# Kernel optimization log

Hardware: AMD Instinct MI355X
Metric: run time of the kernel (lower is better)

The kernel has to match this reference:

```python
import jax, jax.numpy as jnp
import numpy as np

# --- quantization helpers (I-BERT-style symmetric quantization) ---

def _quant_int(x, scale, bit):
    # round(x/scale) clamped to signed `bit`-bit range (SymmetricQuantFunction)
    n = 2 ** (bit - 1) - 1
    return jnp.clip(jnp.round(x / scale), -n - 1, n)


def quant_linear(x, s_x, W, b, weight_bit=8):
    """QuantLinear: per-output-channel symmetric 8-bit weight quant, int GEMM, dequant.
    Returns (output, bias_scaling_factor[out_features])."""
    n = 2 ** (weight_bit - 1) - 1
    w_scale = jnp.maximum(jnp.max(jnp.abs(W), axis=1), 1e-8) / n          # (out,)
    w_int = _quant_int(W, w_scale[:, None], weight_bit)                   # int-valued (out,in)
    b_scale = w_scale * s_x                                               # (out,) broadcasts with scalar s_x
    b_int = jnp.round(b / b_scale)                                        # 32-bit bias, no clamp needed
    x_int = x / s_x                                                       # int-valued activations
    out_int = jnp.einsum('bsi,oi->bso', x_int, w_int) + b_int
    return out_int * b_scale, b_scale


def quant_act(x, bit):
    """QuantAct: per-tensor symmetric requantization to `bit` bits (dynamic min/max)."""
    n = 2 ** (bit - 1) - 1
    scale = jnp.maximum(jnp.max(jnp.abs(x)), 1e-8) / n                    # scalar
    x_int = _quant_int(x, scale, bit)
    return x_int * scale, scale


def int_gelu(x, s):
    """IntGELU (I-BERT): integer 2nd-order polynomial approximation of erf."""
    k = 1.4142
    c0, c1 = -0.2888, -1.769
    c2 = 1.0 / c0
    SHIFT = 14  # 'const' in the original code

    x_int = x / s
    se = s / k  # scaling factor fed to int_erf
    # --- int_erf ---
    b_int = jnp.floor(c1 / se)
    c_int = jnp.floor(c2 / se ** 2)
    sign = jnp.sign(x_int)
    abs_int = jnp.minimum(jnp.abs(x_int), -b_int)
    y_int = sign * ((abs_int + b_int) ** 2 + c_int)
    se2 = se ** 2 * c0
    y_int = jnp.floor(y_int / 2 ** SHIFT)
    se2 = se2 * 2 ** SHIFT
    # --- gelu = x * (erf/2 + 1/2) in integer form ---
    shift_int = jnp.floor(1.0 / se2)
    out_int = x_int * (y_int + shift_int)
    s_out = s * se2 / 2
    return out_int * s_out, s_out


def setup_inputs() -> dict:
    key = jax.random.key(0)
    k_x, k_w1, k_b1, k_w2, k_b2 = jax.random.split(key, 5)
    B, S, D, H = 8, 1024, 768, 3072
    x = jax.random.normal(k_x, (B, S, D), dtype=jnp.float32)
    act_scaling_factor = jnp.full((1,), 0.02, dtype=jnp.float32)
    # pre-quantize x onto its input grid (x arrives already quantized in the real pipeline)
    x = jnp.round(x / act_scaling_factor) * act_scaling_factor
    W1 = jax.random.normal(k_w1, (H, D), dtype=jnp.float32) * 0.02
    b1 = jax.random.normal(k_b1, (H,), dtype=jnp.float32) * 0.02
    W2 = jax.random.normal(k_w2, (D, H), dtype=jnp.float32) * 0.02
    b2 = jax.random.normal(k_b2, (D,), dtype=jnp.float32) * 0.02
    return {"x": x, "act_scaling_factor": act_scaling_factor,
            "W1": W1, "b1": b1, "W2": W2, "b2": b2}


def reference(x, act_scaling_factor, W1, b1, W2, b2):
    s = act_scaling_factor
    h, s = quant_linear(x, s, W1, b1)       # fc1: int8 GEMM + dequant
    h, s = quant_act(h, 8)                  # qact_gelu
    h, s = int_gelu(h, s)                   # IntGELU
    h, s = quant_act(h, 8)                  # qact1 (drop=0.0 -> identity)
    h, s = quant_linear(h, s, W2, b2)       # fc2
    h, s = quant_act(h, 16)                 # qact2 (16-bit)
    return h, s
```

## Files before the change

### kernel.cpp

```cpp
#include <hip/hip_runtime.h>

typedef _Float16 half8  __attribute__((ext_vector_type(8)));
typedef _Float16 half4v __attribute__((ext_vector_type(4)));
typedef float f32x4 __attribute__((ext_vector_type(4)));
typedef int int4v __attribute__((ext_vector_type(4)));

#define M_DIM 8192
#define D_DIM 768
#define H_DIM 3072

#define WS_WSCALE2   16
#define WS_BINT1     (WS_WSCALE2 + 768*4)
#define WS_BSCALE1   (WS_BINT1 + 3072*4)
#define WS_BINT2     (WS_BSCALE1 + 3072*4)
#define WS_BSCALE2   (WS_BINT2 + 768*4)
#define WS_XQ        34560UL
#define WS_WQ1       (WS_XQ  + (size_t)M_DIM*D_DIM*2)
#define WS_WQ2I      (WS_WQ1 + (size_t)H_DIM*D_DIM*2)
#define WS_H1        (WS_WQ2I + (size_t)D_DIM*H_DIM)
#define WS_Q2        WS_H1
#define WS_H2        (WS_H1 + (size_t)M_DIM*H_DIM)
#define WS_Q1        (WS_H1 + (size_t)M_DIM*H_DIM*4)

__device__ __forceinline__ void gl_lds16(const _Float16* g, _Float16* l) {
  __builtin_amdgcn_global_load_lds(
      (const __attribute__((address_space(1))) void*)g,
      (__attribute__((address_space(3))) void*)l, 16, 0, 0);
}
__device__ __forceinline__ void gl_lds16c(const char* g, char* l) {
  __builtin_amdgcn_global_load_lds(
      (const __attribute__((address_space(1))) void*)g,
      (__attribute__((address_space(3))) void*)l, 16, 0, 0);
}

struct GeluP { float scale1, bintg, cintg, shiftint, s_out; };

__device__ __forceinline__ GeluP gelu_params(float max1) {
  GeluP p;
  p.scale1 = fmaxf(max1, 1e-8f) / 127.0f;
  float se = p.scale1 / 1.4142f;
  p.bintg = floorf(-1.769f / se);
  p.cintg = floorf(((float)(1.0 / -0.2888)) / (se * se));
  float se2 = ((se * se) * -0.2888f) * 16384.0f;
  p.shiftint = floorf(1.0f / se2);
  p.s_out = (p.scale1 * se2) * 0.5f;
  return p;
}

__device__ __forceinline__ float gelu_val(const GeluP& p, float qf) {
  float sg = (qf > 0.f) ? 1.f : ((qf < 0.f) ? -1.f : 0.f);
  float aq = fminf(fabsf(qf), -p.bintg);
  float t = aq + p.bintg;
  float y = sg * (t * t + p.cintg);
  float yf = floorf(y * (1.0f / 16384.0f));
  return (qf * (yf + p.shiftint)) * p.s_out;
}

__global__ __launch_bounds__(256)
void k1_prep(const float* __restrict__ W1, const float* __restrict__ b1,
             const float* __restrict__ W2, const float* __restrict__ sxp,
             _Float16* __restrict__ wq1, char* __restrict__ wq2i,
             float* __restrict__ wscale2, float* __restrict__ bint1,
             float* __restrict__ bscale1, unsigned* __restrict__ wsu)
{
  if (blockIdx.x == 0 && threadIdx.x == 0) { wsu[0] = 0u; wsu[1] = 0u; wsu[2] = 0u; }
  int w = blockIdx.x * 4 + (threadIdx.x >> 6);
  int lane = threadIdx.x & 63;
  if (w < H_DIM) {
    const float* row = W1 + (size_t)w * D_DIM;
    f32x4 v[3]; float m = 0.f;
#pragma unroll
    for (int t = 0; t < 3; t++) {
      v[t] = *(const f32x4*)(row + t * 256 + lane * 4);
#pragma unroll
      for (int j = 0; j < 4; j++) m = fmaxf(m, fabsf(v[t][j]));
    }
#pragma unroll
    for (int off = 32; off >= 1; off >>= 1) m = fmaxf(m, __shfl_xor(m, off));
    float wsc = fmaxf(m, 1e-8f) / 127.0f;
    _Float16* orow = wq1 + (size_t)w * D_DIM;
#pragma unroll
    for (int t = 0; t < 3; t++) {
      half4v h;
#pragma unroll
      for (int j = 0; j < 4; j++) {
        float q = fminf(fmaxf(rintf(v[t][j] / wsc), -128.f), 127.f);
        h[j] = (_Float16)q;
      }
      *(half4v*)(orow + t * 256 + lane * 4) = h;
    }
    if (lane == 0) {
      float bs = wsc * sxp[0];
      bint1[w] = rintf(b1[w] / bs);
      bscale1[w] = bs;
    }
  } else {
    int o = w - H_DIM;
    const float* row = W2 + (size_t)o * H_DIM;
    f32x4 v[12]; float m = 0.f;
#pragma unroll
    for (int t = 0; t < 12; t++) {
      v[t] = *(const f32x4*)(row + t * 256 + lane * 4);
#pragma unroll
      for (int j = 0; j < 4; j++) m = fmaxf(m, fabsf(v[t][j]));
    }
#pragma unroll
    for (int off = 32; off >= 1; off >>= 1) m = fmaxf(m, __shfl_xor(m, off));
    float wsc = fmaxf(m, 1e-8f) / 127.0f;
    unsigned* orow = (unsigned*)(wq2i + (size_t)o * H_DIM);
#pragma unroll
    for (int t = 0; t < 12; t++) {
      unsigned pk = 0;
#pragma unroll
      for (int j = 0; j < 4; j++) {
        float q = fminf(fmaxf(rintf(v[t][j] / wsc), -128.f), 127.f);
        pk |= ((unsigned)(unsigned char)(char)(int)q) << (8 * j);
      }
      orow[t * 64 + lane] = pk;
    }
    if (lane == 0) wscale2[o] = wsc;
  }
}

__global__ __launch_bounds__(256)
void k2_quant_x(const float* __restrict__ x, const float* __restrict__ sxp,
                _Float16* __restrict__ xq, int n4)
{
  float sx = sxp[0];
  int stride = gridDim.x * blockDim.x;
  for (int i = blockIdx.x * blockDim.x + threadIdx.x; i < n4; i += stride) {
    f32x4 v = ((const f32x4*)x)[i];
    half4v h;
#pragma unroll
    for (int j = 0; j < 4; j++) h[j] = (_Float16)(v[j] / sx);
    ((half4v*)xq)[i] = h;
  }
}

#define SLOT_A 4096
#define SLOT_B 8192
#define SLOT_SZ (SLOT_A + SLOT_B)

__global__ __launch_bounds__(512)
void gemm_f16_dp(const _Float16* __restrict__ A, const _Float16* __restrict__ B,
                 const float* __restrict__ bint, const float* __restrict__ bscale,
                 float* __restrict__ C, unsigned* __restrict__ maxw, int N, int K)
{
  __shared__ _Float16 lds[3 * SLOT_SZ];
  __shared__ float wred[8];
  const int tid = threadIdx.x;
  const int wid = tid >> 6;
  const int lane = tid & 63;
  const int m0 = blockIdx.x * 128;
  const int n0 = blockIdx.y * 256;
  const int wm = wid >> 2;
  const int wn = wid & 3;

  const int sr = lane >> 2;
  const int sc = lane & 3;
  const int ra  = wid * 16 + sr;
  const int csa = sc ^ ((ra >> 1) & 3);
  const int rb  = wid * 16 + sr;
  const int csb = sc ^ ((rb >> 1) & 3);
  const _Float16* pa  = A + (size_t)(m0 + ra) * K + csa * 8;
  const _Float16* pb0 = B + (size_t)(n0 + rb) * K + csb * 8;
  const _Float16* pb1 = B + (size_t)(n0 + rb + 128) * K + csb * 8;
  _Float16* const da  = lds;
  _Float16* const db0 = lds + SLOT_A;
  _Float16* const db1 = lds + SLOT_A + 4096;

#define STAGE_DP(t, s) do {                                                  \
    const int _o = (s) * SLOT_SZ + wid * 512;                                \
    gl_lds16(pa  + (size_t)(t) * 32, da  + _o);                              \
    gl_lds16(pb0 + (size_t)(t) * 32, db0 + _o);                              \
    gl_lds16(pb1 + (size_t)(t) * 32, db1 + _o);                              \
  } while (0)

  int aoff[4], boff[4];
  const int ks = lane >> 4;
#pragma unroll
  for (int f = 0; f < 4; f++) {
    int r = wm * 64 + f * 16 + (lane & 15);
    aoff[f] = r * 64 + ((ks ^ ((r >> 1) & 3)) * 16);
    int rn = wn * 64 + f * 16 + (lane & 15);
    boff[f] = SLOT_A * 2 + rn * 64 + ((ks ^ ((rn >> 1) & 3)) * 16);
  }

  f32x4 acc[4][4];
#pragma unroll
  for (int i = 0; i < 4; i++)
#pragma unroll
    for (int j = 0; j < 4; j++) acc[i][j] = (f32x4){0.f, 0.f, 0.f, 0.f};

  const int nt = K / 32;
  STAGE_DP(0, 0);
  STAGE_DP(1, 1);
  for (int t = 0; t < nt; ++t) {
    const int s = t % 3;
    if (t + 1 < nt) asm volatile("s_waitcnt vmcnt(3)" ::: "memory");
    else            asm volatile("s_waitcnt vmcnt(0)" ::: "memory");
    __builtin_amdgcn_s_barrier();
    if (t + 2 < nt) STAGE_DP(t + 2, (t + 2) % 3);
    const char* sb = (const char*)(lds + s * SLOT_SZ);
    half8 a[4], b[4];
#pragma unroll
    for (int f = 0; f < 4; f++) a[f] = *(const half8*)(sb + aoff[f]);
#pragma unroll
    for (int f = 0; f < 4; f++) b[f] = *(const half8*)(sb + boff[f]);
    asm volatile("s_waitcnt lgkmcnt(0)" ::: "memory");
    __builtin_amdgcn_sched_barrier(0);
    __builtin_amdgcn_s_setprio(1);
#pragma unroll
    for (int i = 0; i < 4; i++)
#pragma unroll
      for (int j = 0; j < 4; j++)
        acc[i][j] = __builtin_amdgcn_mfma_f32_16x16x32_f16(a[i], b[j], acc[i][j], 0, 0, 0);
    __builtin_amdgcn_s_setprio(0);
  }
#undef STAGE_DP

  float tmax = 0.f;
  const int orow0 = m0 + wm * 64 + (lane >> 4) * 4;
  const int ocol0 = n0 + wn * 64 + (lane & 15);
#pragma unroll
  for (int j = 0; j < 4; j++) {
    const int col = ocol0 + j * 16;
    const float bi = bint[col];
    const float bs = bscale[col];
#pragma unroll
    for (int i = 0; i < 4; i++) {
#pragma unroll
      for (int e = 0; e < 4; e++) {
        const int rowm = orow0 + i * 16 + e;
        float v = (acc[i][j][e] + bi) * bs;
        C[(size_t)rowm * N + col] = v;
        tmax = fmaxf(tmax, fabsf(v));
      }
    }
  }
#pragma unroll
  for (int off = 32; off >= 1; off >>= 1) tmax = fmaxf(tmax, __shfl_xor(tmax, off));
  if (lane == 0) wred[wid] = tmax;
  __syncthreads();
  if (tid == 0) {
    float bm = 0.f;
#pragma unroll
    for (int i = 0; i < 8; i++) bm = fmaxf(bm, wred[i]);
    atomicMax(maxw, __float_as_uint(bm));
  }
}

__global__ __launch_bounds__(256)
void k4_gelu(const float* __restrict__ h1, const unsigned* __restrict__ wsu,
             char* __restrict__ q1, unsigned* __restrict__ maxw, int n4)
{
  GeluP p = gelu_params(__uint_as_float(wsu[0]));
  float tmax = 0.f;
  int stride = gridDim.x * blockDim.x;
  for (int i = blockIdx.x * blockDim.x + threadIdx.x; i < n4; i += stride) {
    f32x4 h = ((const f32x4*)h1)[i];
    unsigned pack = 0;
#pragma unroll
    for (int j = 0; j < 4; j++) {
      float qf = fminf(fmaxf(rintf(h[j] / p.scale1), -128.f), 127.f);
      tmax = fmaxf(tmax, fabsf(gelu_val(p, qf)));
      pack |= ((unsigned)(unsigned char)(char)(int)qf) << (8 * j);
    }
    ((unsigned*)q1)[i] = pack;
  }
#pragma unroll
  for (int off = 32; off >= 1; off >>= 1) tmax = fmaxf(tmax, __shfl_xor(tmax, off));
  __shared__ float wred[4];
  int wid = threadIdx.x >> 6;
  if ((threadIdx.x & 63) == 0) wred[wid] = tmax;
  __syncthreads();
  if (threadIdx.x == 0) {
    float bm = fmaxf(fmaxf(wred[0], wred[1]), fmaxf(wred[2], wred[3]));
    atomicMax(maxw, __float_as_uint(bm));
  }
}

__global__ __launch_bounds__(256)
void k6_bias(const unsigned* __restrict__ wsu, const float* __restrict__ wscale2,
             const float* __restrict__ b2, float* __restrict__ bint2,
             float* __restrict__ bscale2)
{
  float scale2 = fmaxf(__uint_as_float(wsu[1]), 1e-8f) / 127.0f;
  for (int o = threadIdx.x; o < D_DIM; o += 256) {
    float bs = wscale2[o] * scale2;
    bint2[o] = rintf(b2[o] / bs);
    bscale2[o] = bs;
  }
}

__global__ __launch_bounds__(256)
void k5_q2(const char* __restrict__ q1, const unsigned* __restrict__ wsu,
           char* __restrict__ q2, int n16)
{
  GeluP p = gelu_params(__uint_as_float(wsu[0]));
  float scale2 = fmaxf(__uint_as_float(wsu[1]), 1e-8f) / 127.0f;
  int stride = gridDim.x * blockDim.x;
  for (int i = blockIdx.x * blockDim.x + threadIdx.x; i < n16; i += stride) {
    uint4 pk = ((const uint4*)q1)[i];
    uint4 o;
    unsigned* pw[4] = {&o.x, &o.y, &o.z, &o.w};
    unsigned pr[4] = {pk.x, pk.y, pk.z, pk.w};
#pragma unroll
    for (int w = 0; w < 4; w++) {
      unsigned acc = 0;
#pragma unroll
      for (int j = 0; j < 4; j++) {
        float qf = (float)(int)(signed char)(pr[w] >> (8 * j));
        float g = gelu_val(p, qf);
        float q2f = fminf(fmaxf(rintf(g / scale2), -128.f), 127.f);
        acc |= ((unsigned)(unsigned char)(char)(int)q2f) << (8 * j);
      }
      *pw[w] = acc;
    }
    ((uint4*)q2)[i] = o;
  }
}

__global__ __launch_bounds__(256)
void gemm_i8(const char* __restrict__ A, const char* __restrict__ B,
             const float* __restrict__ bint, const float* __restrict__ bscale,
             float* __restrict__ C, unsigned* __restrict__ maxw, int N, int K)
{
  __shared__ char sA[2][64 * 64];
  __shared__ char sB[2][128 * 64];
  __shared__ float wred[4];
  const int tid = threadIdx.x;
  const int wid = tid >> 6;
  const int lane = tid & 63;
  const int m0 = blockIdx.x * 64;
  const int n0 = blockIdx.y * 128;
  const int wr = (wid >> 1) * 32;
  const int wc = (wid & 1) * 64;
  const int lrow = lane & 15;
  const int lkc = (lane >> 4) * 16;
  const int srow = lane >> 2;
  const int schunk = (lane & 3) * 16;

  const char* Ab = A + (size_t)m0 * K;
  const char* Bb = B + (size_t)n0 * K;

  int4v acc[2][4];
#pragma unroll
  for (int i = 0; i < 2; i++)
#pragma unroll
    for (int j = 0; j < 4; j++) acc[i][j] = (int4v){0, 0, 0, 0};

  const int nt = K / 64;

#define STAGE_I8(bufi, k0) do {                                               \
    char* dA = sA[bufi]; char* dB = sB[bufi];                                 \
    gl_lds16c(Ab + (size_t)(wid * 16 + srow) * K + ((k0) + schunk),           \
              dA + wid * 1024);                                               \
    _Pragma("unroll")                                                         \
    for (int r = 0; r < 2; r++) {                                             \
      const int rq = r * 4 + wid;                                             \
      gl_lds16c(Bb + (size_t)(rq * 16 + srow) * K + ((k0) + schunk),          \
                dB + rq * 1024);                                              \
    } } while (0)

  STAGE_I8(0, 0);
  __syncthreads();
  int cur = 0;
  for (int t = 0; t < nt; ++t) {
    if (t + 1 < nt) STAGE_I8(cur ^ 1, (t + 1) * 64);
    int4v a[2], b[4];
#pragma unroll
    for (int f = 0; f < 2; f++)
      a[f] = *(const int4v*)&sA[cur][(wr + f * 16 + lrow) * 64 + lkc];
#pragma unroll
    for (int f = 0; f < 4; f++)
      b[f] = *(const int4v*)&sB[cur][(wc + f * 16 + lrow) * 64 + lkc];
#pragma unroll
    for (int i = 0; i < 2; i++)
#pragma unroll
      for (int j = 0; j < 4; j++)
        acc[i][j] = __builtin_amdgcn_mfma_i32_16x16x64_i8(a[i], b[j], acc[i][j], 0, 0, 0);
    __syncthreads();
    cur ^= 1;
  }
#undef STAGE_I8

  float tmax = 0.f;
  const int orow0 = m0 + wr + (lane >> 4) * 4;
  const int ocol0 = n0 + wc + lrow;
#pragma unroll
  for (int j = 0; j < 4; j++) {
    const int col = ocol0 + j * 16;
    const float bi = bint[col];
    const float bs = bscale[col];
#pragma unroll
    for (int i = 0; i < 2; i++) {
#pragma unroll
      for (int e = 0; e < 4; e++) {
        const int rowm = orow0 + i * 16 + e;
        float v = ((float)acc[i][j][e] + bi) * bs;
        C[(size_t)rowm * N + col] = v;
        tmax = fmaxf(tmax, fabsf(v));
      }
    }
  }
#pragma unroll
  for (int off = 32; off >= 1; off >>= 1) tmax = fmaxf(tmax, __shfl_xor(tmax, off));
  if (lane == 0) wred[wid] = tmax;
  __syncthreads();
  if (tid == 0) {
    float bm = fmaxf(fmaxf(wred[0], wred[1]), fmaxf(wred[2], wred[3]));
    atomicMax(maxw, __float_as_uint(bm));
  }
}

__global__ __launch_bounds__(256)
void k7_final(const float* __restrict__ h2, const unsigned* __restrict__ wsu,
              float* __restrict__ out, int n4, int ntot)
{
  float scale16 = fmaxf(__uint_as_float(wsu[2]), 1e-8f) / 32767.0f;
  int stride = gridDim.x * blockDim.x;
  for (int i = blockIdx.x * blockDim.x + threadIdx.x; i < n4; i += stride) {
    f32x4 v = ((const f32x4*)h2)[i];
    f32x4 o;
#pragma unroll
    for (int j = 0; j < 4; j++) {
      float q = fminf(fmaxf(rintf(v[j] / scale16), -32768.f), 32767.f);
      o[j] = q * scale16;
    }
    ((f32x4*)out)[i] = o;
  }
  if (blockIdx.x == 0 && threadIdx.x == 0) out[ntot] = scale16;
}

extern "C" void kernel_launch(void* const* d_in, const int* in_sizes, int n_in,
                              void* d_out, int out_size, void* d_ws, size_t ws_size,
                              hipStream_t stream)
{
  (void)in_sizes; (void)n_in; (void)out_size; (void)ws_size;
  const float* x  = (const float*)d_in[0];
  const float* sx = (const float*)d_in[1];
  const float* W1 = (const float*)d_in[2];
  const float* b1 = (const float*)d_in[3];
  const float* W2 = (const float*)d_in[4];
  const float* b2 = (const float*)d_in[5];
  float* out = (float*)d_out;
  char* ws = (char*)d_ws;

  unsigned* wsu   = (unsigned*)ws;
  float* wscale2  = (float*)(ws + WS_WSCALE2);
  float* bint1    = (float*)(ws + WS_BINT1);
  float* bscale1  = (float*)(ws + WS_BSCALE1);
  float* bint2    = (float*)(ws + WS_BINT2);
  float* bscale2  = (float*)(ws + WS_BSCALE2);
  _Float16* xq    = (_Float16*)(ws + WS_XQ);
  _Float16* wq1   = (_Float16*)(ws + WS_WQ1);
  char* wq2i      = (char*)(ws + WS_WQ2I);
  float* h1       = (float*)(ws + WS_H1);
  char* q2        = (char*)(ws + WS_Q2);
  float* h2       = (float*)(ws + WS_H2);
  char* q1        = (char*)(ws + WS_Q1);

  k1_prep<<<dim3(960), dim3(256), 0, stream>>>(W1, b1, W2, sx, wq1, wq2i, wscale2, bint1, bscale1, wsu);
  k2_quant_x<<<dim3(2048), dim3(256), 0, stream>>>(x, sx, xq, (M_DIM * D_DIM) / 4);
  gemm_f16_dp<<<dim3(64, 12), dim3(512), 0, stream>>>(xq, wq1, bint1, bscale1, h1, wsu + 0, H_DIM, D_DIM);
  k4_gelu<<<dim3(2048), dim3(256), 0, stream>>>(h1, wsu, q1, wsu + 1, (M_DIM * H_DIM) / 4);
  k6_bias<<<dim3(1), dim3(256), 0, stream>>>(wsu, wscale2, b2, bint2, bscale2);
  k5_q2<<<dim3(2048), dim3(256), 0, stream>>>(q1, wsu, q2, (M_DIM * H_DIM) / 16);
  gemm_i8<<<dim3(128, 6), dim3(256), 0, stream>>>(q2, wq2i, bint2, bscale2, h2, wsu + 2, D_DIM, H_DIM);
  k7_final<<<dim3(2048), dim3(256), 0, stream>>>(h2, wsu, out, (M_DIM * D_DIM) / 4, M_DIM * D_DIM);
}
```

Measured before the change: 186.8 us.

## Rewrite int8 GEMM with triple-buffered LDS pipeline and larger tiles

Replaces the double-buffered 64x128 int8 fc2 GEMM with a 128x128-tile kernel that uses three LDS slots, two tiles of prefetch with vmcnt-based waits, and an XOR swizzle on the LDS layout to avoid bank conflicts. It also splits the B-fragment LDS reads into two halves interleaved with MFMA groups, in both the int8 and the f16 GEMM. The goal is to hide global load latency, raise data reuse per block, and overlap LDS reads with MFMA. The cost is more registers and LDS per block and half as many blocks (384), which may limit occupancy and leave some CUs idle on the 256-CU part.

```diff
diff --git a/kernel.cpp b/kernel.cpp
--- a/kernel.cpp
+++ b/kernel.cpp
@@ -199,22 +199,29 @@
     const int s = t % 3;
     if (t + 1 < nt) asm volatile("s_waitcnt vmcnt(3)" ::: "memory");
     else            asm volatile("s_waitcnt vmcnt(0)" ::: "memory");
-    __builtin_amdgcn_s_barrier();
+    asm volatile("s_barrier" ::: "memory");
     if (t + 2 < nt) STAGE_DP(t + 2, (t + 2) % 3);
     const char* sb = (const char*)(lds + s * SLOT_SZ);
-    half8 a[4], b[4];
+    half8 a[4], b01[2], b23[2];
 #pragma unroll
     for (int f = 0; f < 4; f++) a[f] = *(const half8*)(sb + aoff[f]);
-#pragma unroll
-    for (int f = 0; f < 4; f++) b[f] = *(const half8*)(sb + boff[f]);
-    asm volatile("s_waitcnt lgkmcnt(0)" ::: "memory");
-    __builtin_amdgcn_sched_barrier(0);
+    b01[0] = *(const half8*)(sb + boff[0]);
+    b01[1] = *(const half8*)(sb + boff[1]);
     __builtin_amdgcn_s_setprio(1);
 #pragma unroll
     for (int i = 0; i < 4; i++)
 #pragma unroll
-      for (int j = 0; j < 4; j++)
-        acc[i][j] = __builtin_amdgcn_mfma_f32_16x16x32_f16(a[i], b[j], acc[i][j], 0, 0, 0);
+      for (int j = 0; j < 2; j++)
+        acc[i][j] = __builtin_amdgcn_mfma_f32_16x16x32_f16(a[i], b01[j], acc[i][j], 0, 0, 0);
+    __builtin_amdgcn_s_setprio(0);
+    b23[0] = *(const half8*)(sb + boff[2]);
+    b23[1] = *(const half8*)(sb + boff[3]);
+    __builtin_amdgcn_s_setprio(1);
+#pragma unroll
+    for (int i = 0; i < 4; i++)
+#pragma unroll
+      for (int j = 0; j < 2; j++)
+        acc[i][j + 2] = __builtin_amdgcn_mfma_f32_16x16x32_f16(a[i], b23[j], acc[i][j + 2], 0, 0, 0);
     __builtin_amdgcn_s_setprio(0);
   }
 #undef STAGE_DP
@@ -321,80 +328,103 @@
   }
 }
 
-__global__ __launch_bounds__(256)
-void gemm_i8(const char* __restrict__ A, const char* __restrict__ B,
-             const float* __restrict__ bint, const float* __restrict__ bscale,
-             float* __restrict__ C, unsigned* __restrict__ maxw, int N, int K)
-{
-  __shared__ char sA[2][64 * 64];
-  __shared__ char sB[2][128 * 64];
+#define I8_SLOT_A 8192
+#define I8_SLOT_SZ (2 * I8_SLOT_A)
+
+__global__ __launch_bounds__(256)
+void gemm_i8_dp(const char* __restrict__ A, const char* __restrict__ B,
+                const float* __restrict__ bint, const float* __restrict__ bscale,
+                float* __restrict__ C, unsigned* __restrict__ maxw, int N, int K)
+{
+  __shared__ char lds[3 * I8_SLOT_SZ];
   __shared__ float wred[4];
   const int tid = threadIdx.x;
   const int wid = tid >> 6;
   const int lane = tid & 63;
-  const int m0 = blockIdx.x * 64;
+  const int m0 = blockIdx.x * 128;
   const int n0 = blockIdx.y * 128;
-  const int wr = (wid >> 1) * 32;
-  const int wc = (wid & 1) * 64;
-  const int lrow = lane & 15;
-  const int lkc = (lane >> 4) * 16;
-  const int srow = lane >> 2;
-  const int schunk = (lane & 3) * 16;
-
-  const char* Ab = A + (size_t)m0 * K;
-  const char* Bb = B + (size_t)n0 * K;
-
-  int4v acc[2][4];
-#pragma unroll
-  for (int i = 0; i < 2; i++)
+  const int wm = wid >> 1;
+  const int wn = wid & 1;
+
+  const int rr = lane >> 2;
+  const int c  = lane & 3;
+  const int r0 = wid * 16 + rr;
+  const int r1 = r0 + 64;
+  const int c0 = c ^ (r0 & 3) ^ ((r0 >> 2) & 3);
+  const int c1 = c ^ (r1 & 3) ^ ((r1 >> 2) & 3);
+  const char* pa0 = A + (size_t)(m0 + r0) * K + c0 * 16;
+  const char* pa1 = A + (size_t)(m0 + r1) * K + c1 * 16;
+  const char* pb0 = B + (size_t)(n0 + r0) * K + c0 * 16;
+  const char* pb1 = B + (size_t)(n0 + r1) * K + c1 * 16;
+
+#define STAGE_I8(t, s) do {                                                   \
+    char* const base = lds + (s) * I8_SLOT_SZ;                                \
+    gl_lds16c(pa0 + (size_t)(t) * 64, base + wid * 1024);                     \
+    gl_lds16c(pa1 + (size_t)(t) * 64, base + 4096 + wid * 1024);              \
+    gl_lds16c(pb0 + (size_t)(t) * 64, base + I8_SLOT_A + wid * 1024);         \
+    gl_lds16c(pb1 + (size_t)(t) * 64, base + I8_SLOT_A + 4096 + wid * 1024);  \
+  } while (0)
+
+  int aoff[4], boff[4];
+  const int ks = lane >> 4;
+#pragma unroll
+  for (int f = 0; f < 4; f++) {
+    int r = wm * 64 + f * 16 + (lane & 15);
+    aoff[f] = r * 64 + ((ks ^ (r & 3) ^ ((r >> 2) & 3)) * 16);
+    int rn = wn * 64 + f * 16 + (lane & 15);
+    boff[f] = I8_SLOT_A + rn * 64 + ((ks ^ (rn & 3) ^ ((rn >> 2) & 3)) * 16);
+  }
+
+  int4v acc[4][4];
+#pragma unroll
+  for (int i = 0; i < 4; i++)
 #pragma unroll
     for (int j = 0; j < 4; j++) acc[i][j] = (int4v){0, 0, 0, 0};
 
   const int nt = K / 64;
-
-#define STAGE_I8(bufi, k0) do {                                               \
-    char* dA = sA[bufi]; char* dB = sB[bufi];                                 \
-    gl_lds16c(Ab + (size_t)(wid * 16 + srow) * K + ((k0) + schunk),           \
-              dA + wid * 1024);                                               \
-    _Pragma("unroll")                                                         \
-    for (int r = 0; r < 2; r++) {                                             \
-      const int rq = r * 4 + wid;                                             \
-      gl_lds16c(Bb + (size_t)(rq * 16 + srow) * K + ((k0) + schunk),          \
-                dB + rq * 1024);                                              \
-    } } while (0)
-
   STAGE_I8(0, 0);
-  __syncthreads();
-  int cur = 0;
+  STAGE_I8(1, 1);
   for (int t = 0; t < nt; ++t) {
-    if (t + 1 < nt) STAGE_I8(cur ^ 1, (t + 1) * 64);
-    int4v a[2], b[4];
-#pragma unroll
-    for (int f = 0; f < 2; f++)
-      a[f] = *(const int4v*)&sA[cur][(wr + f * 16 + lrow) * 64 + lkc];
-#pragma unroll
-    for (int f = 0; f < 4; f++)
-      b[f] = *(const int4v*)&sB[cur][(wc + f * 16 + lrow) * 64 + lkc];
-#pragma unroll
-    for (int i = 0; i < 2; i++)
-#pragma unroll
-      for (int j = 0; j < 4; j++)
-        acc[i][j] = __builtin_amdgcn_mfma_i32_16x16x64_i8(a[i], b[j], acc[i][j], 0, 0, 0);
-    __syncthreads();
-    cur ^= 1;
+    const int s = t % 3;
+    if (t + 1 < nt) asm volatile("s_waitcnt vmcnt(4)" ::: "memory");
+    else            asm volatile("s_waitcnt vmcnt(0)" ::: "memory");
+    asm volatile("s_barrier" ::: "memory");
+    if (t + 2 < nt) STAGE_I8(t + 2, (t + 2) % 3);
+    const char* sb = lds + s * I8_SLOT_SZ;
+    int4v a[4], b01[2], b23[2];
+#pragma unroll
+    for (int f = 0; f < 4; f++) a[f] = *(const int4v*)(sb + aoff[f]);
+    b01[0] = *(const int4v*)(sb + boff[0]);
+    b01[1] = *(const int4v*)(sb + boff[1]);
+    __builtin_amdgcn_s_setprio(1);
+#pragma unroll
+    for (int i = 0; i < 4; i++)
+#pragma unroll
+      for (int j = 0; j < 2; j++)
+        acc[i][j] = __builtin_amdgcn_mfma_i32_16x16x64_i8(a[i], b01[j], acc[i][j], 0, 0, 0);
+    __builtin_amdgcn_s_setprio(0);
+    b23[0] = *(const int4v*)(sb + boff[2]);
+    b23[1] = *(const int4v*)(sb + boff[3]);
+    __builtin_amdgcn_s_setprio(1);
+#pragma unroll
+    for (int i = 0; i < 4; i++)
+#pragma unroll
+      for (int j = 0; j < 2; j++)
+        acc[i][j + 2] = __builtin_amdgcn_mfma_i32_16x16x64_i8(a[i], b23[j], acc[i][j + 2], 0, 0, 0);
+    __builtin_amdgcn_s_setprio(0);
   }
 #undef STAGE_I8
 
   float tmax = 0.f;
-  const int orow0 = m0 + wr + (lane >> 4) * 4;
-  const int ocol0 = n0 + wc + lrow;
+  const int orow0 = m0 + wm * 64 + (lane >> 4) * 4;
+  const int ocol0 = n0 + wn * 64 + (lane & 15);
 #pragma unroll
   for (int j = 0; j < 4; j++) {
     const int col = ocol0 + j * 16;
     const float bi = bint[col];
     const float bs = bscale[col];
 #pragma unroll
-    for (int i = 0; i < 2; i++) {
+    for (int i = 0; i < 4; i++) {
 #pragma unroll
       for (int e = 0; e < 4; e++) {
         const int rowm = orow0 + i * 16 + e;
@@ -467,6 +497,6 @@
   k4_gelu<<<dim3(2048), dim3(256), 0, stream>>>(h1, wsu, q1, wsu + 1, (M_DIM * H_DIM) / 4);
   k6_bias<<<dim3(1), dim3(256), 0, stream>>>(wsu, wscale2, b2, bint2, bscale2);
   k5_q2<<<dim3(2048), dim3(256), 0, stream>>>(q1, wsu, q2, (M_DIM * H_DIM) / 16);
-  gemm_i8<<<dim3(128, 6), dim3(256), 0, stream>>>(q2, wq2i, bint2, bscale2, h2, wsu + 2, D_DIM, H_DIM);
+  gemm_i8_dp<<<dim3(64, 6), dim3(256), 0, stream>>>(q2, wq2i, bint2, bscale2, h2, wsu + 2, D_DIM, H_DIM);
   k7_final<<<dim3(2048), dim3(256), 0, stream>>>(h2, wsu, out, (M_DIM * D_DIM) / 4, M_DIM * D_DIM);
 }
```

Result: no change. 183.4 us (-1.8%).
